# Kernel optimization log

Measured on AMD Instinct MI355X. Metric: run time of the kernel, lower is better.

## Reference

```python
import jax, jax.numpy as jnp
import numpy as np

N, IN_C, HID, OUT_C = 100000, 512, 256, 32
E = 1_600_000
K, LAM1, LAM2 = 5, 3.0, 3.0  # elastic prop hyperparams


def setup_inputs() -> dict:
    key = jax.random.key(0)
    ks = jax.random.split(key, 6)
    x = jax.random.normal(ks[0], (N, IN_C), dtype=jnp.float32)
    edge_index = jax.random.randint(ks[1], (2, E), 0, N, dtype=jnp.int64)
    s1 = 1.0 / np.sqrt(IN_C)
    s2 = 1.0 / np.sqrt(HID)
    W1 = jax.random.uniform(ks[2], (IN_C, HID), jnp.float32, -s1, s1)
    b1 = jax.random.uniform(ks[3], (HID,), jnp.float32, -s1, s1)
    W2 = jax.random.uniform(ks[4], (HID, OUT_C), jnp.float32, -s2, s2)
    b2 = jax.random.uniform(ks[5], (OUT_C,), jnp.float32, -s2, s2)
    return dict(x=x, edge_index=edge_index, W1=W1, b1=b1, W2=W2, b2=b2)


def _emp(h, row, col):
    """Elastic Message Passing (ElasticGNN): proximal-gradient iterations over
    the degree-normalized incidence operator with L1 dual projection."""
    n = h.shape[0]
    deg = jnp.zeros((n,), h.dtype).at[row].add(1.0).at[col].add(1.0)
    dis = jax.lax.rsqrt(jnp.maximum(deg, 1.0))  # 1/sqrt(deg)
    dr = dis[row][:, None]  # [E,1]
    dc = dis[col][:, None]
    gamma = 1.0 / (1.0 + LAM2)
    beta = 1.0 / (2.0 * gamma)

    def step(carry, _):
        z, y = carry
        # dual ascent on edge variables: z += beta * (Delta y), then project
        # onto the L-inf ball of radius lambda1 (prox of L1 penalty's dual)
        z = jnp.clip(z + beta * (y[row] * dr - y[col] * dc), -LAM1, LAM1)
        # primal: y = gamma * h - gamma * Delta^T z  (scatter back to nodes)
        atz = jnp.zeros_like(y).at[row].add(z * dr).at[col].add(-(z * dc))
        y = gamma * h - gamma * atz
        return (z, y), None

    z0 = jnp.zeros((row.shape[0], h.shape[1]), h.dtype)
    (z, y), _ = jax.lax.scan(step, (z0, gamma * h), None, length=K)
    return y


def reference(x, edge_index, W1, b1, W2, b2):
    # eval mode: dropout is identity
    h = jax.nn.relu(x @ W1 + b1)
    h = h @ W2 + b2                       # [N, OUT_C]
    row, col = edge_index[0], edge_index[1]
    y = _emp(h, row, col)                 # sparse elastic propagation
    return jax.nn.log_softmax(y, axis=1)
```

## Files before the change

### kernel.cpp

```cpp
#include <hip/hip_runtime.h>
#include <math.h>

#define IN_C  512
#define HID   256
#define OUT_C 32
#define GAMMA 0.25f
#define BETA  2.0f
#define LAM1  3.0f
#define ZS    10922.0f
#define ZSI   (1.0f / 10922.0f)

#define BM 128
#define BN 128
#define BK 16

__global__ __launch_bounds__(256) void gemm1_relu_kernel(
    const float* __restrict__ A, const float* __restrict__ B,
    const float* __restrict__ bias, float* __restrict__ C, int M)
{
    __shared__ float As[BK][BM + 4];
    __shared__ float Bs[BK][BN + 4];
    const int tid = threadIdx.x;
    const int bm = blockIdx.x * BM;
    const int bn = blockIdx.y * BN;
    const int tx = tid & 15;
    const int ty = tid >> 4;

    float acc[8][8];
#pragma unroll
    for (int i = 0; i < 8; ++i)
#pragma unroll
        for (int j = 0; j < 8; ++j) acc[i][j] = 0.f;

    const int a_row = tid >> 2;
    const int a_col = (tid & 3) << 2;
    const int b_row = tid >> 5;
    const int b_col = (tid & 31) << 2;

    for (int k0 = 0; k0 < IN_C; k0 += BK) {
#pragma unroll
        for (int r = 0; r < 2; ++r) {
            const int m = a_row + r * 64;
            const int gm = bm + m;
            float4 v = make_float4(0.f, 0.f, 0.f, 0.f);
            if (gm < M) v = *(const float4*)&A[(size_t)gm * IN_C + k0 + a_col];
            As[a_col + 0][m] = v.x;
            As[a_col + 1][m] = v.y;
            As[a_col + 2][m] = v.z;
            As[a_col + 3][m] = v.w;
        }
#pragma unroll
        for (int r = 0; r < 2; ++r) {
            const int kk = b_row + r * 8;
            *(float4*)&Bs[kk][b_col] =
                *(const float4*)&B[(size_t)(k0 + kk) * HID + bn + b_col];
        }
        __syncthreads();
#pragma unroll
        for (int kk = 0; kk < BK; ++kk) {
            float a[8], b[8];
            *(float4*)&a[0] = *(float4*)&As[kk][ty * 8];
            *(float4*)&a[4] = *(float4*)&As[kk][ty * 8 + 4];
            *(float4*)&b[0] = *(float4*)&Bs[kk][tx * 4];
            *(float4*)&b[4] = *(float4*)&Bs[kk][64 + tx * 4];
#pragma unroll
            for (int i = 0; i < 8; ++i)
#pragma unroll
                for (int j = 0; j < 8; ++j)
                    acc[i][j] = fmaf(a[i], b[j], acc[i][j]);
        }
        __syncthreads();
    }

#pragma unroll
    for (int i = 0; i < 8; ++i) {
        const int gm = bm + ty * 8 + i;
        if (gm >= M) continue;
#pragma unroll
        for (int g = 0; g < 2; ++g) {
            const int gn = bn + g * 64 + tx * 4;
            float4 v;
            v.x = fmaxf(acc[i][g * 4 + 0] + bias[gn + 0], 0.f);
            v.y = fmaxf(acc[i][g * 4 + 1] + bias[gn + 1], 0.f);
            v.z = fmaxf(acc[i][g * 4 + 2] + bias[gn + 2], 0.f);
            v.w = fmaxf(acc[i][g * 4 + 3] + bias[gn + 3], 0.f);
            *(float4*)&C[(size_t)gm * HID + gn] = v;
        }
    }
}

#define G2_ROWS 128
#define G2_KT   64

__global__ __launch_bounds__(256) void gemm2_kernel(
    const float* __restrict__ H1, const float* __restrict__ W2,
    const float* __restrict__ b2, float* __restrict__ H,
    float* __restrict__ Y, int M)
{
    __shared__ float W2s[HID * OUT_C];
    __shared__ float rows_s[G2_ROWS][G2_KT + 4];
    const int tid = threadIdx.x;
    const int brow = blockIdx.x * G2_ROWS;
    const int cg = tid & 7;
    const int rg = tid >> 3;

#pragma unroll
    for (int r = 0; r < 8; ++r)
        ((float4*)W2s)[tid + r * 256] = ((const float4*)W2)[tid + r * 256];

    float acc[4][4];
#pragma unroll
    for (int r = 0; r < 4; ++r)
#pragma unroll
        for (int c = 0; c < 4; ++c) acc[r][c] = 0.f;

    for (int k0 = 0; k0 < HID; k0 += G2_KT) {
        __syncthreads();
#pragma unroll
        for (int i = 0; i < 8; ++i) {
            const int idx = tid + i * 256;
            const int rl = idx >> 4;
            const int c4 = idx & 15;
            const int gr = brow + rl;
            float4 v = make_float4(0.f, 0.f, 0.f, 0.f);
            if (gr < M) v = *(const float4*)&H1[(size_t)gr * HID + k0 + c4 * 4];
            *(float4*)&rows_s[rl][c4 * 4] = v;
        }
        __syncthreads();
#pragma unroll
        for (int kq = 0; kq < G2_KT / 4; ++kq) {
            float4 w[4];
#pragma unroll
            for (int j = 0; j < 4; ++j)
                w[j] = ((const float4*)W2s)[(k0 + kq * 4 + j) * 8 + cg];
#pragma unroll
            for (int r = 0; r < 4; ++r) {
                const float4 rh = *(const float4*)&rows_s[rg * 4 + r][kq * 4];
                acc[r][0] = fmaf(rh.x, w[0].x, acc[r][0]);
                acc[r][1] = fmaf(rh.x, w[0].y, acc[r][1]);
                acc[r][2] = fmaf(rh.x, w[0].z, acc[r][2]);
                acc[r][3] = fmaf(rh.x, w[0].w, acc[r][3]);
                acc[r][0] = fmaf(rh.y, w[1].x, acc[r][0]);
                acc[r][1] = fmaf(rh.y, w[1].y, acc[r][1]);
                acc[r][2] = fmaf(rh.y, w[1].z, acc[r][2]);
                acc[r][3] = fmaf(rh.y, w[1].w, acc[r][3]);
                acc[r][0] = fmaf(rh.z, w[2].x, acc[r][0]);
                acc[r][1] = fmaf(rh.z, w[2].y, acc[r][1]);
                acc[r][2] = fmaf(rh.z, w[2].z, acc[r][2]);
                acc[r][3] = fmaf(rh.z, w[2].w, acc[r][3]);
                acc[r][0] = fmaf(rh.w, w[3].x, acc[r][0]);
                acc[r][1] = fmaf(rh.w, w[3].y, acc[r][1]);
                acc[r][2] = fmaf(rh.w, w[3].z, acc[r][2]);
                acc[r][3] = fmaf(rh.w, w[3].w, acc[r][3]);
            }
        }
    }

    const float4 bias = *(const float4*)&b2[cg * 4];
#pragma unroll
    for (int r = 0; r < 4; ++r) {
        const int grow = brow + rg * 4 + r;
        if (grow >= M) continue;
        float4 s;
        s.x = acc[r][0] + bias.x;
        s.y = acc[r][1] + bias.y;
        s.z = acc[r][2] + bias.z;
        s.w = acc[r][3] + bias.w;
        *(float4*)&H[(size_t)grow * OUT_C + cg * 4] = s;
        float4 y0;
        y0.x = GAMMA * s.x; y0.y = GAMMA * s.y;
        y0.z = GAMMA * s.z; y0.w = GAMMA * s.w;
        *(float4*)&Y[(size_t)grow * OUT_C + cg * 4] = y0;
    }
}

__global__ void hist2_kernel(const int* __restrict__ row, const int* __restrict__ col,
                             int* __restrict__ cnt_r, int* __restrict__ cnt_c, int E)
{
    const int t = blockIdx.x * blockDim.x + threadIdx.x;
    if (t >= E) return;
    atomicAdd(&cnt_r[row[t]], 1);
    atomicAdd(&cnt_c[col[t]], 1);
}

__global__ void dis_kernel(const int* __restrict__ cnt_r, const int* __restrict__ cnt_c,
                           float* __restrict__ dis, int N)
{
    const int t = blockIdx.x * blockDim.x + threadIdx.x;
    if (t < N) dis[t] = 1.f / sqrtf(fmaxf((float)(cnt_r[t] + cnt_c[t]), 1.f));
}

#define SCAN_CHUNK 1024

__global__ __launch_bounds__(256) void scan1_kernel(
    const int* __restrict__ counts, int* __restrict__ bsum, int N)
{
    __shared__ int sm[256];
    const int tid = threadIdx.x;
    const int base = blockIdx.x * SCAN_CHUNK + tid * 4;
    int s = 0;
#pragma unroll
    for (int i = 0; i < 4; ++i)
        if (base + i < N) s += counts[base + i];
    sm[tid] = s;
    __syncthreads();
    for (int off = 128; off; off >>= 1) {
        if (tid < off) sm[tid] += sm[tid + off];
        __syncthreads();
    }
    if (tid == 0) bsum[blockIdx.x] = sm[0];
}

__global__ void scan2_kernel(int* __restrict__ bsum, int* __restrict__ boff, int nb)
{
    if (threadIdx.x == 0 && blockIdx.x == 0) {
        int acc = 0;
        for (int i = 0; i < nb; ++i) { boff[i] = acc; acc += bsum[i]; }
    }
}

__global__ __launch_bounds__(256) void scan3_kernel(
    const int* __restrict__ counts, const int* __restrict__ boff,
    int* __restrict__ ptr, int* __restrict__ cursor, int N)
{
    __shared__ int sm[256];
    const int tid = threadIdx.x;
    const int base = blockIdx.x * SCAN_CHUNK + tid * 4;
    int c[4];
#pragma unroll
    for (int i = 0; i < 4; ++i)
        c[i] = (base + i < N) ? counts[base + i] : 0;
    const int tsum = c[0] + c[1] + c[2] + c[3];
    sm[tid] = tsum;
    __syncthreads();
    for (int off = 1; off < 256; off <<= 1) {
        int v = (tid >= off) ? sm[tid - off] : 0;
        __syncthreads();
        sm[tid] += v;
        __syncthreads();
    }
    int run = boff[blockIdx.x] + sm[tid] - tsum;
#pragma unroll
    for (int i = 0; i < 4; ++i) {
        if (base + i < N) {
            ptr[base + i] = run;
            cursor[base + i] = run;
        }
        run += c[i];
    }
}

__global__ void scatter2_kernel(const int* __restrict__ row, const int* __restrict__ col,
                                int* __restrict__ cur_r, int* __restrict__ cur_c,
                                int* __restrict__ col_s, int* __restrict__ row_s, int E)
{
    const int t = blockIdx.x * blockDim.x + threadIdx.x;
    if (t >= E) return;
    const int r = row[t], c = col[t];
    const int nid = atomicAdd(&cur_r[r], 1);
    col_s[nid] = c;
    const int pc = atomicAdd(&cur_c[c], 1);
    row_s[pc] = r;
}

__device__ __forceinline__ float clip1(float v)
{
    return fminf(fmaxf(v, -LAM1), LAM1);
}

__device__ __forceinline__ float4 zload4(const short* p)
{
    const short4 s = *(const short4*)p;
    return make_float4(s.x * ZSI, s.y * ZSI, s.z * ZSI, s.w * ZSI);
}

__device__ __forceinline__ void zstore4(short* p, float4 z)
{
    short4 s;
    s.x = (short)__float2int_rn(z.x * ZS);
    s.y = (short)__float2int_rn(z.y * ZS);
    s.z = (short)__float2int_rn(z.z * ZS);
    s.w = (short)__float2int_rn(z.w * ZS);
    *(short4*)p = s;
}

template <bool FIRST, bool LAST>
__global__ __launch_bounds__(256) void emp_kernel(
    const int* __restrict__ rowptr, const int* __restrict__ cnt_r,
    const int* __restrict__ col_s,
    const int* __restrict__ colptr, const int* __restrict__ cnt_c,
    const int* __restrict__ row_s,
    short* __restrict__ zr, short* __restrict__ zc,
    const float* __restrict__ dis, const float* __restrict__ H,
    const float* __restrict__ Yold, float* __restrict__ Ynew,
    float* __restrict__ OUT, int N)
{
    const int t = blockIdx.x * 256 + threadIdx.x;
    const int n = t >> 3;
    if (n >= N) return;
    const int c4 = (t & 7) << 2;
    const float dn = dis[n];
    const float4 ys = *(const float4*)&Yold[(size_t)n * OUT_C + c4];
    const float4 ysdn = make_float4(ys.x * dn, ys.y * dn, ys.z * dn, ys.w * dn);

    float4 acc = make_float4(0.f, 0.f, 0.f, 0.f);

    {
        const int b = rowptr[n];
        const int d = cnt_r[n];
        for (int i = 0; i < d; ++i) {
            const int e = b + i;
            const int other = col_s[e];
            const float dt = dis[other];
            const float4 yo = *(const float4*)&Yold[(size_t)other * OUT_C + c4];
            float4 z;
            if (FIRST) z = make_float4(0.f, 0.f, 0.f, 0.f);
            else       z = zload4(&zr[(size_t)e * OUT_C + c4]);
            z.x = clip1(z.x + BETA * (ysdn.x - yo.x * dt));
            z.y = clip1(z.y + BETA * (ysdn.y - yo.y * dt));
            z.z = clip1(z.z + BETA * (ysdn.z - yo.z * dt));
            z.w = clip1(z.w + BETA * (ysdn.w - yo.w * dt));
            acc.x += z.x; acc.y += z.y; acc.z += z.z; acc.w += z.w;
            if (!LAST) zstore4(&zr[(size_t)e * OUT_C + c4], z);
        }
    }

    {
        const int b = colptr[n];
        const int d = cnt_c[n];
        for (int i = 0; i < d; ++i) {
            const int p = b + i;
            const int other = row_s[p];
            const float dt = dis[other];
            const float4 yo = *(const float4*)&Yold[(size_t)other * OUT_C + c4];
            float4 z;
            if (FIRST) z = make_float4(0.f, 0.f, 0.f, 0.f);
            else       z = zload4(&zc[(size_t)p * OUT_C + c4]);
            z.x = clip1(z.x + BETA * (yo.x * dt - ysdn.x));
            z.y = clip1(z.y + BETA * (yo.y * dt - ysdn.y));
            z.z = clip1(z.z + BETA * (yo.z * dt - ysdn.z));
            z.w = clip1(z.w + BETA * (yo.w * dt - ysdn.w));
            acc.x -= z.x; acc.y -= z.y; acc.z -= z.z; acc.w -= z.w;
            if (!LAST) zstore4(&zc[(size_t)p * OUT_C + c4], z);
        }
    }

    const float4 h4 = *(const float4*)&H[(size_t)n * OUT_C + c4];
    float4 v;
    v.x = GAMMA * (h4.x - dn * acc.x);
    v.y = GAMMA * (h4.y - dn * acc.y);
    v.z = GAMMA * (h4.z - dn * acc.z);
    v.w = GAMMA * (h4.w - dn * acc.w);

    if (!LAST) {
        *(float4*)&Ynew[(size_t)n * OUT_C + c4] = v;
    } else {
        float m = fmaxf(fmaxf(v.x, v.y), fmaxf(v.z, v.w));
#pragma unroll
        for (int off = 4; off; off >>= 1) m = fmaxf(m, __shfl_xor(m, off, 8));
        float sum = expf(v.x - m) + expf(v.y - m) + expf(v.z - m) + expf(v.w - m);
#pragma unroll
        for (int off = 4; off; off >>= 1) sum += __shfl_xor(sum, off, 8);
        const float lse = m + logf(sum);
        float4 o;
        o.x = v.x - lse; o.y = v.y - lse; o.z = v.z - lse; o.w = v.w - lse;
        *(float4*)&OUT[(size_t)n * OUT_C + c4] = o;
    }
}

extern "C" void kernel_launch(void* const* d_in, const int* in_sizes, int n_in,
                              void* d_out, int out_size, void* d_ws, size_t ws_size,
                              hipStream_t stream)
{
    const float* x  = (const float*)d_in[0];
    const int*   ei = (const int*)d_in[1];
    const float* W1 = (const float*)d_in[2];
    const float* b1 = (const float*)d_in[3];
    const float* W2 = (const float*)d_in[4];
    const float* b2 = (const float*)d_in[5];
    const int M = in_sizes[0] / IN_C;
    const int E = in_sizes[1] / 2;
    const int* row = ei;
    const int* col = ei + E;

    char* ws = (char*)d_ws;
    short* zr = (short*)ws;
    short* zc = zr + (size_t)E * OUT_C;
    float* h1 = (float*)ws;
    float* h  = (float*)(zc + (size_t)E * OUT_C);
    float* y0 = h  + (size_t)M * OUT_C;
    float* y1 = y0 + (size_t)M * OUT_C;
    int* cnt_r   = (int*)(y1 + (size_t)M * OUT_C);
    int* cnt_c   = cnt_r + M;
    int* rowptr  = cnt_c + M;
    int* colptr  = rowptr + M;
    int* cur_r   = colptr + M;
    int* cur_c   = cur_r + M;
    float* dis   = (float*)(cur_c + M);
    const int nb = (M + SCAN_CHUNK - 1) / SCAN_CHUNK;
    int* bsum    = (int*)(dis + M);
    int* boff    = bsum + nb;
    int* col_s   = boff + nb;
    int* row_s   = col_s + E;

    hipMemsetAsync(cnt_r, 0, 2 * (size_t)M * sizeof(int), stream);

    dim3 g1((M + BM - 1) / BM, HID / BN);
    gemm1_relu_kernel<<<g1, 256, 0, stream>>>(x, W1, b1, h1, M);
    gemm2_kernel<<<(M + G2_ROWS - 1) / G2_ROWS, 256, 0, stream>>>(h1, W2, b2, h, y0, M);

    hist2_kernel<<<(E + 255) / 256, 256, 0, stream>>>(row, col, cnt_r, cnt_c, E);
    dis_kernel<<<(M + 255) / 256, 256, 0, stream>>>(cnt_r, cnt_c, dis, M);
    scan1_kernel<<<nb, 256, 0, stream>>>(cnt_r, bsum, M);
    scan2_kernel<<<1, 64, 0, stream>>>(bsum, boff, nb);
    scan3_kernel<<<nb, 256, 0, stream>>>(cnt_r, boff, rowptr, cur_r, M);
    scan1_kernel<<<nb, 256, 0, stream>>>(cnt_c, bsum, M);
    scan2_kernel<<<1, 64, 0, stream>>>(bsum, boff, nb);
    scan3_kernel<<<nb, 256, 0, stream>>>(cnt_c, boff, colptr, cur_c, M);
    scatter2_kernel<<<(E + 255) / 256, 256, 0, stream>>>(row, col, cur_r, cur_c,
                                                         col_s, row_s, E);

    const int nblocks = (M * 8 + 255) / 256;
    emp_kernel<true, false><<<nblocks, 256, 0, stream>>>(
        rowptr, cnt_r, col_s, colptr, cnt_c, row_s,
        zr, zc, dis, h, y0, y1, nullptr, M);
    emp_kernel<false, false><<<nblocks, 256, 0, stream>>>(
        rowptr, cnt_r, col_s, colptr, cnt_c, row_s,
        zr, zc, dis, h, y1, y0, nullptr, M);
    emp_kernel<false, false><<<nblocks, 256, 0, stream>>>(
        rowptr, cnt_r, col_s, colptr, cnt_c, row_s,
        zr, zc, dis, h, y0, y1, nullptr, M);
    emp_kernel<false, false><<<nblocks, 256, 0, stream>>>(
        rowptr, cnt_r, col_s, colptr, cnt_c, row_s,
        zr, zc, dis, h, y1, y0, nullptr, M);
    emp_kernel<false, true><<<nblocks, 256, 0, stream>>>(
        rowptr, cnt_r, col_s, colptr, cnt_c, row_s,
        zr, zc, dis, h, y0, nullptr, (float*)d_out, M);
}
```

Baseline: 1.720 ms.

## Run first GEMM on bf16 MFMA with split hi/lo emulation of fp32

Replaces the scalar-FMA fp32 GEMM for x@W1 with a matrix-core kernel. Each fp32 operand is split into bf16 high and low parts, and three bf16 MFMAs (hh, hl, lh) per tile approximate fp32 accuracy. A small pre-kernel converts and transposes W1 into hi/lo bf16 buffers in the workspace. This cuts the ALU cost of the largest GEMM in exchange for in-kernel conversion of x, and it drops the lo*lo term, which slightly reduces precision.

Result: faster. 1.668 ms (-3.0%).

```diff
diff --git a/kernel.cpp b/kernel.cpp
--- a/kernel.cpp
+++ b/kernel.cpp
@@ -10,81 +10,129 @@
 #define ZS    10922.0f
 #define ZSI   (1.0f / 10922.0f)
 
-#define BM 128
-#define BN 128
-#define BK 16
-
-__global__ __launch_bounds__(256) void gemm1_relu_kernel(
-    const float* __restrict__ A, const float* __restrict__ B,
-    const float* __restrict__ bias, float* __restrict__ C, int M)
-{
-    __shared__ float As[BK][BM + 4];
-    __shared__ float Bs[BK][BN + 4];
+__device__ __forceinline__ unsigned short f2bf(float f)
+{
+    unsigned u = __float_as_uint(f);
+    return (unsigned short)((u + 0x7fffu + ((u >> 16) & 1u)) >> 16);
+}
+__device__ __forceinline__ float bf2f(unsigned short h)
+{
+    return __uint_as_float(((unsigned)h) << 16);
+}
+
+__global__ __launch_bounds__(256) void wconv_kernel(
+    const float* __restrict__ W1, unsigned short* __restrict__ WhT,
+    unsigned short* __restrict__ WlT)
+{
+    const int t = blockIdx.x * 256 + threadIdx.x;
+    const int k = t >> 8;
+    const int n = t & 255;
+    const float w = W1[t];
+    const unsigned short h = f2bf(w);
+    const unsigned short l = f2bf(w - bf2f(h));
+    WhT[n * 512 + k] = h;
+    WlT[n * 512 + k] = l;
+}
+
+typedef __attribute__((ext_vector_type(8))) short bf16x8;
+typedef __attribute__((ext_vector_type(4))) float f32x4;
+
+#define PITCH 40
+
+__global__ __launch_bounds__(256) void gemm1_mfma_kernel(
+    const float* __restrict__ X, const unsigned short* __restrict__ WhT,
+    const unsigned short* __restrict__ WlT, const float* __restrict__ bias,
+    float* __restrict__ C, int M)
+{
+    __shared__ __align__(16) unsigned short Ah[128 * PITCH];
+    __shared__ __align__(16) unsigned short Al[128 * PITCH];
+    __shared__ __align__(16) unsigned short Bh[128 * PITCH];
+    __shared__ __align__(16) unsigned short Bl[128 * PITCH];
+
     const int tid = threadIdx.x;
-    const int bm = blockIdx.x * BM;
-    const int bn = blockIdx.y * BN;
-    const int tx = tid & 15;
-    const int ty = tid >> 4;
-
-    float acc[8][8];
-#pragma unroll
-    for (int i = 0; i < 8; ++i)
-#pragma unroll
-        for (int j = 0; j < 8; ++j) acc[i][j] = 0.f;
-
-    const int a_row = tid >> 2;
-    const int a_col = (tid & 3) << 2;
-    const int b_row = tid >> 5;
-    const int b_col = (tid & 31) << 2;
-
-    for (int k0 = 0; k0 < IN_C; k0 += BK) {
-#pragma unroll
-        for (int r = 0; r < 2; ++r) {
-            const int m = a_row + r * 64;
-            const int gm = bm + m;
+    const int bm = blockIdx.x * 128;
+    const int bn = blockIdx.y * 128;
+    const int lane = tid & 63;
+    const int wid = tid >> 6;
+    const int wm = (wid >> 1) * 64;
+    const int wn = (wid & 1) * 64;
+    const int l16 = lane & 15;
+    const int l4 = lane >> 4;
+
+    f32x4 acc[4][4];
+#pragma unroll
+    for (int i = 0; i < 4; ++i)
+#pragma unroll
+        for (int j = 0; j < 4; ++j) acc[i][j] = (f32x4){0.f, 0.f, 0.f, 0.f};
+
+    for (int k0 = 0; k0 < IN_C; k0 += 32) {
+#pragma unroll
+        for (int p = 0; p < 4; ++p) {
+            const int idx = tid + p * 256;
+            const int r = idx >> 3;
+            const int f4 = idx & 7;
             float4 v = make_float4(0.f, 0.f, 0.f, 0.f);
-            if (gm < M) v = *(const float4*)&A[(size_t)gm * IN_C + k0 + a_col];
-            As[a_col + 0][m] = v.x;
-            As[a_col + 1][m] = v.y;
-            As[a_col + 2][m] = v.z;
-            As[a_col + 3][m] = v.w;
-        }
-#pragma unroll
-        for (int r = 0; r < 2; ++r) {
-            const int kk = b_row + r * 8;
-            *(float4*)&Bs[kk][b_col] =
-                *(const float4*)&B[(size_t)(k0 + kk) * HID + bn + b_col];
-        }
-        __syncthreads();
-#pragma unroll
-        for (int kk = 0; kk < BK; ++kk) {
-            float a[8], b[8];
-            *(float4*)&a[0] = *(float4*)&As[kk][ty * 8];
-            *(float4*)&a[4] = *(float4*)&As[kk][ty * 8 + 4];
-            *(float4*)&b[0] = *(float4*)&Bs[kk][tx * 4];
-            *(float4*)&b[4] = *(float4*)&Bs[kk][64 + tx * 4];
-#pragma unroll
-            for (int i = 0; i < 8; ++i)
-#pragma unroll
-                for (int j = 0; j < 8; ++j)
-                    acc[i][j] = fmaf(a[i], b[j], acc[i][j]);
-        }
-        __syncthreads();
-    }
-
-#pragma unroll
-    for (int i = 0; i < 8; ++i) {
-        const int gm = bm + ty * 8 + i;
-        if (gm >= M) continue;
-#pragma unroll
-        for (int g = 0; g < 2; ++g) {
-            const int gn = bn + g * 64 + tx * 4;
-            float4 v;
-            v.x = fmaxf(acc[i][g * 4 + 0] + bias[gn + 0], 0.f);
-            v.y = fmaxf(acc[i][g * 4 + 1] + bias[gn + 1], 0.f);
-            v.z = fmaxf(acc[i][g * 4 + 2] + bias[gn + 2], 0.f);
-            v.w = fmaxf(acc[i][g * 4 + 3] + bias[gn + 3], 0.f);
-            *(float4*)&C[(size_t)gm * HID + gn] = v;
+            if (bm + r < M)
+                v = *(const float4*)&X[(size_t)(bm + r) * IN_C + k0 + f4 * 4];
+            const unsigned short h0 = f2bf(v.x), h1 = f2bf(v.y),
+                                 h2 = f2bf(v.z), h3 = f2bf(v.w);
+            const unsigned short l0 = f2bf(v.x - bf2f(h0)),
+                                 l1 = f2bf(v.y - bf2f(h1)),
+                                 l2 = f2bf(v.z - bf2f(h2)),
+                                 l3 = f2bf(v.w - bf2f(h3));
+            *(short4*)&Ah[r * PITCH + f4 * 4] =
+                make_short4((short)h0, (short)h1, (short)h2, (short)h3);
+            *(short4*)&Al[r * PITCH + f4 * 4] =
+                make_short4((short)l0, (short)l1, (short)l2, (short)l3);
+        }
+#pragma unroll
+        for (int p = 0; p < 2; ++p) {
+            const int idx = tid + p * 256;
+            const int r = idx >> 2;
+            const int ch = idx & 3;
+            const size_t g = (size_t)(bn + r) * IN_C + k0 + ch * 8;
+            *(int4*)&Bh[r * PITCH + ch * 8] = *(const int4*)&WhT[g];
+            *(int4*)&Bl[r * PITCH + ch * 8] = *(const int4*)&WlT[g];
+        }
+        __syncthreads();
+
+        bf16x8 ah[4], al[4];
+#pragma unroll
+        for (int i = 0; i < 4; ++i) {
+            const int arow = wm + i * 16 + l16;
+            ah[i] = *(const bf16x8*)&Ah[arow * PITCH + l4 * 8];
+            al[i] = *(const bf16x8*)&Al[arow * PITCH + l4 * 8];
+        }
+#pragma unroll
+        for (int j = 0; j < 4; ++j) {
+            const int bcol = wn + j * 16 + l16;
+            const bf16x8 bh = *(const bf16x8*)&Bh[bcol * PITCH + l4 * 8];
+            const bf16x8 bl = *(const bf16x8*)&Bl[bcol * PITCH + l4 * 8];
+#pragma unroll
+            for (int i = 0; i < 4; ++i) {
+                acc[i][j] = __builtin_amdgcn_mfma_f32_16x16x32_bf16(
+                    ah[i], bh, acc[i][j], 0, 0, 0);
+                acc[i][j] = __builtin_amdgcn_mfma_f32_16x16x32_bf16(
+                    ah[i], bl, acc[i][j], 0, 0, 0);
+                acc[i][j] = __builtin_amdgcn_mfma_f32_16x16x32_bf16(
+                    al[i], bh, acc[i][j], 0, 0, 0);
+            }
+        }
+        __syncthreads();
+    }
+
+#pragma unroll
+    for (int j = 0; j < 4; ++j) {
+        const int col = bn + wn + j * 16 + l16;
+        const float bv = bias[col];
+#pragma unroll
+        for (int i = 0; i < 4; ++i) {
+#pragma unroll
+            for (int r = 0; r < 4; ++r) {
+                const int row = bm + wm + i * 16 + l4 * 4 + r;
+                if (row < M)
+                    C[(size_t)row * HID + col] = fmaxf(acc[i][j][r] + bv, 0.f);
+            }
         }
     }
 }
@@ -402,11 +450,14 @@
     int* boff    = bsum + nb;
     int* col_s   = boff + nb;
     int* row_s   = col_s + E;
+    unsigned short* W1hT = (unsigned short*)(row_s + E);
+    unsigned short* W1lT = W1hT + HID * IN_C;
 
     hipMemsetAsync(cnt_r, 0, 2 * (size_t)M * sizeof(int), stream);
 
-    dim3 g1((M + BM - 1) / BM, HID / BN);
-    gemm1_relu_kernel<<<g1, 256, 0, stream>>>(x, W1, b1, h1, M);
+    wconv_kernel<<<IN_C, 256, 0, stream>>>(W1, W1hT, W1lT);
+    dim3 g1((M + 127) / 128, HID / 128);
+    gemm1_mfma_kernel<<<g1, 256, 0, stream>>>(x, W1hT, W1lT, b1, h1, M);
     gemm2_kernel<<<(M + G2_ROWS - 1) / G2_ROWS, 256, 0, stream>>>(h1, W2, b2, h, y0, M);
 
     hist2_kernel<<<(E + 255) / 256, 256, 0, stream>>>(row, col, cnt_r, cnt_c, E);
```
